# Performance work log

Measured on AMD Instinct MI355X. Metric: run time of the kernel, lower is better.

The kernel has to match this reference:

```python
import jax, jax.numpy as jnp
import numpy as np

# NCHW 3x3 conv, padding=1. BatchNorm (inference affine) is folded into conv weight/bias,
# which is mathematically identical to Conv->BN(eval) in the original.
def conv3(x, w, b, stride):
    y = jax.lax.conv_general_dilated(x, w, (stride, stride), [(1, 1), (1, 1)],
                                     dimension_numbers=('NCHW', 'OIHW', 'NCHW'))
    return y + b[None, :, None, None]

def lin1(x, w, b):  # 1x1 conv as channel matmul; w: [out, in]
    return jnp.einsum('oc,bchw->bohw', w, x) + b[None, :, None, None]

def setup_inputs():
    key = jax.random.key(0)
    ks = list(jax.random.split(key, 32))
    C, M = 32, 32  # cv_hypo_num, mid_dim (kq_dim == mid_dim since mid_dim <= 128)
    B, H, W = 1, 256, 512
    w3 = lambda k, o, i: jax.random.normal(k, (o, i, 3, 3), jnp.float32) * 0.05
    w1 = lambda k, o, i: jax.random.normal(k, (o, i), jnp.float32) * 0.05
    bv = lambda k, o: jax.random.normal(k, (o,), jnp.float32) * 0.01
    inp = {
        'mono_pseudo_cost': jax.random.normal(ks[0], (B, C, H, W), jnp.float32),
        'cost_volume': jax.random.normal(ks[1], (B, C, H, W), jnp.float32),
        # mono_expand / multi_expand: two stride-2 conv(+folded BN)+ReLU blocks each
        'me_w1': w3(ks[2], M, C), 'me_b1': bv(ks[3], M),
        'me_w2': w3(ks[4], M, C), 'me_b2': bv(ks[5], M),
        'xe_w1': w3(ks[6], M, C), 'xe_b1': bv(ks[7], M),
        'xe_w2': w3(ks[8], M, C), 'xe_b2': bv(ks[9], M),
        # 1x1 q/k/v projections for both branches
        'mq_w': w1(ks[10], M, M), 'mq_b': bv(ks[11], M),
        'mk_w': w1(ks[12], M, M), 'mk_b': bv(ks[13], M),
        'mv_w': w1(ks[14], M, M), 'mv_b': bv(ks[15], M),
        'xq_w': w1(ks[16], M, M), 'xq_b': bv(ks[17], M),
        'xk_w': w1(ks[18], M, M), 'xk_b': bv(ks[19], M),
        'xv_w': w1(ks[20], M, M), 'xv_b': bv(ks[21], M),
        # residual branches
        'mr_w1': w3(ks[22], M, C), 'mr_b1': bv(ks[23], M),
        'mr_w2': w3(ks[24], M, C), 'mr_b2': bv(ks[25], M),
        'xr_w': w1(ks[26], M, C), 'xr_b': bv(ks[27], M),
        'gamma': jnp.full((1,), 0.5, jnp.float32),  # nonzero so attention path is live
    }
    return inp

def reference(mono_pseudo_cost, cost_volume,
              me_w1, me_b1, me_w2, me_b2,
              xe_w1, xe_b1, xe_w2, xe_b2,
              mq_w, mq_b, mk_w, mk_b, mv_w, mv_b,
              xq_w, xq_b, xk_w, xk_b, xv_w, xv_b,
              mr_w1, mr_b1, mr_w2, mr_b2,
              xr_w, xr_b, gamma):
    relu = jax.nn.relu
    init_h, init_w = cost_volume.shape[2], cost_volume.shape[3]
    M = me_w1.shape[0]
    # feature extractors (stride-2 x2): [B,32,256,512] -> [B,32,64,128]
    mono_feat = relu(conv3(relu(conv3(mono_pseudo_cost, me_w1, me_b1, 2)), me_w2, me_b2, 2))
    multi_feat = relu(conv3(relu(conv3(cost_volume, xe_w1, xe_b1, 2)), xe_w2, xe_b2, 2))
    b, c, h, w = multi_feat.shape
    hw = h * w
    # q/k/v as [B, C, hw]
    mono_q = lin1(mono_feat, mq_w, mq_b).reshape(b, -1, hw)
    mono_k = lin1(mono_feat, mk_w, mk_b).reshape(b, -1, hw)
    mono_v = lin1(mono_feat, mv_w, mv_b).reshape(b, -1, hw)
    multi_q = lin1(multi_feat, xq_w, xq_b).reshape(b, -1, hw)
    multi_k = lin1(multi_feat, xk_w, xk_b).reshape(b, -1, hw)
    multi_v = lin1(multi_feat, xv_w, xv_b).reshape(b, -1, hw)
    # full [B, hw, hw] attention, no 1/sqrt(d) scaling (as in original)
    mono_atten = jax.nn.softmax(jnp.einsum('bci,bcj->bij', mono_q, mono_k), axis=-1)
    multi_atten = jax.nn.softmax(jnp.einsum('bci,bcj->bij', multi_q, multi_k), axis=-1)
    # cross application: mono values weighted by multi attention and vice versa
    mono_out = jnp.einsum('bcj,bij->bci', mono_v, multi_atten).reshape(b, M, h, w)
    multi_out = jnp.einsum('bcj,bij->bci', multi_v, mono_atten).reshape(b, M, h, w)
    fused = jnp.concatenate([multi_out, mono_out], axis=1)
    # nearest-neighbor upsample back to input size (integer factor 4)
    fused = jnp.repeat(jnp.repeat(fused, init_h // h, axis=2), init_w // w, axis=3)
    # residual branches
    mono_residual = relu(conv3(relu(conv3(mono_pseudo_cost, mr_w1, mr_b1, 1)), mr_w2, mr_b2, 1))
    multi_residual = relu(lin1(cost_volume, xr_w, xr_b))
    fused = jnp.concatenate([mono_residual, multi_residual], axis=1) + gamma * fused
    return fused
```

## Files before the change

### kernel.cpp

```cpp
#include <hip/hip_runtime.h>


using bf16x8 = __attribute__((ext_vector_type(8))) short;
using f32x4  = __attribute__((ext_vector_type(4))) float;
using f32x16 = __attribute__((ext_vector_type(16))) float;
typedef unsigned short u16;
typedef unsigned int   u32;

__device__ __forceinline__ u16 f2bf(float f) {
  u32 u = __builtin_bit_cast(u32, f);
  u = (u + 0x7fffu + ((u >> 16) & 1u)) >> 16;
  return (u16)u;
}
__device__ __forceinline__ float bf2f(u16 v) {
  u32 u = ((u32)v) << 16;
  return __builtin_bit_cast(float, u);
}
__device__ __forceinline__ u32 pktr(float lo, float hi) {
  return __builtin_amdgcn_perm(__builtin_bit_cast(u32, hi),
                               __builtin_bit_cast(u32, lo), 0x07060302u);
}
__device__ __forceinline__ f32x4 mfma16(bf16x8 a, bf16x8 b, f32x4 c) {
  return __builtin_amdgcn_mfma_f32_16x16x32_bf16(a, b, c, 0, 0, 0);
}
__device__ __forceinline__ f32x16 mfma32(bf16x8 a, bf16x8 b, f32x16 c) {
  return __builtin_amdgcn_mfma_f32_32x32x16_bf16(a, b, c, 0, 0, 0);
}
__device__ __forceinline__ f32x16 zero16() {
  f32x16 z = {0,0,0,0,0,0,0,0,0,0,0,0,0,0,0,0};
  return z;
}
__device__ __forceinline__ void store4bf(u16* dst, f32x4 v) {
  u32 lo = (u32)f2bf(v[0]) | ((u32)f2bf(v[1]) << 16);
  u32 hi = (u32)f2bf(v[2]) | ((u32)f2bf(v[3]) << 16);
  *(uint2*)dst = make_uint2(lo, hi);
}

struct WPtrs { const float* p[13]; };

__global__ void k_pre(WPtrs wp, u16* __restrict__ wConv, u16* __restrict__ w1x1,
                      const float* __restrict__ mono, const float* __restrict__ cv,
                      u16* __restrict__ monoT, u16* __restrict__ cvT,
                      u16* __restrict__ m1T, u16* __restrict__ x1T, u16* __restrict__ r1T) {
  int bx = blockIdx.x, t = threadIdx.x;
  if (bx < 13) {
    if (bx < 6) {
      const float* s = wp.p[bx];
      u16* d = wConv + bx * 9216;
      for (int i = t; i < 9216; i += 256) {
        int tap = i >> 10, co = (i >> 5) & 31, ci = i & 31;
        d[i] = f2bf(s[co * 288 + ci * 9 + tap]);
      }
    } else {
      const float* s = wp.p[bx];
      u16* d = w1x1 + (bx - 6) * 1024;
      for (int i = t; i < 1024; i += 256) d[i] = f2bf(s[i]);
    }
    return;
  }
  if (bx < 138) {
    int zb = bx - 13;
    int buf = zb % 5, blk = zb / 5;
    u16* b; int Hp, Wp;
    switch (buf) {
      case 0: b = monoT; Hp = 258; Wp = 514; break;
      case 1: b = cvT;   Hp = 258; Wp = 514; break;
      case 2: b = m1T;   Hp = 130; Wp = 258; break;
      case 3: b = x1T;   Hp = 130; Wp = 258; break;
      default: b = r1T;  Hp = 258; Wp = 514; break;
    }
    int id = blk * 256 + t;
    int cell = id >> 2, c8 = (id & 3) << 3;
    if (cell >= 2 * (Hp + Wp)) return;
    int r, c;
    if (cell < Wp)              { r = 0;                 c = cell; }
    else if (cell < 2 * Wp)     { r = Hp - 1;            c = cell - Wp; }
    else if (cell < 2 * Wp + Hp){ r = cell - 2 * Wp;     c = 0; }
    else                        { r = cell - 2 * Wp - Hp; c = Wp - 1; }
    bf16x8 z = {0, 0, 0, 0, 0, 0, 0, 0};
    *(bf16x8*)&b[(r * Wp + c) * 32 + c8] = z;
    return;
  }
  int idx = bx - 138;
  int xb = idx & 7, y = (idx >> 3) & 255, z = idx >> 11;
  const float* src = z ? cv : mono;
  u16* dst = z ? cvT : monoT;
  int x0 = xb << 6;
  __shared__ u16 tile[64][40];
  int ci = t >> 3, kx = (t & 7) << 3;
  const float* sp = src + ci * 131072 + y * 512 + x0 + kx;
  float4 a = *(const float4*)sp;
  float4 bb = *(const float4*)(sp + 4);
  tile[kx + 0][ci] = f2bf(a.x); tile[kx + 1][ci] = f2bf(a.y);
  tile[kx + 2][ci] = f2bf(a.z); tile[kx + 3][ci] = f2bf(a.w);
  tile[kx + 4][ci] = f2bf(bb.x); tile[kx + 5][ci] = f2bf(bb.y);
  tile[kx + 6][ci] = f2bf(bb.z); tile[kx + 7][ci] = f2bf(bb.w);
  __syncthreads();
  int x = t >> 2, c8 = (t & 3) << 3;
  bf16x8 v = *(bf16x8*)&tile[x][c8];
  *(bf16x8*)(dst + ((y + 1) * 514 + (x0 + x + 1)) * 32 + c8) = v;
}

__device__ __forceinline__ void conv3x3_body(int bxl, int tid,
    const u16* __restrict__ inT, int Wp, const u16* __restrict__ w9,
    const float* __restrict__ bias, u16* __restrict__ out, int outPitch,
    int outOff, int Ho, int tprShift, int stride) {
  int wid = (bxl * 256 + tid) >> 6;
  int lane = tid & 63, ln = lane & 15, q = lane >> 4;
  int y = wid >> tprShift;
  int x0 = (wid & ((1 << tprShift) - 1)) << 4;
  if (y >= Ho) return;
  f32x4 acc0 = *(const f32x4*)(bias + q * 4);
  f32x4 acc1 = *(const f32x4*)(bias + 16 + q * 4);
  const u16* ib = inT + (stride * y * Wp + stride * (x0 + ln)) * 32 + q * 8;
  const u16* wb = w9 + ln * 32 + q * 8;
#pragma unroll
  for (int dy = 0; dy < 3; ++dy)
#pragma unroll
    for (int dx = 0; dx < 3; ++dx) {
      int tap = dy * 3 + dx;
      bf16x8 bf = *(const bf16x8*)(ib + (dy * Wp + dx) * 32);
      acc0 = mfma16(*(const bf16x8*)(wb + tap * 1024), bf, acc0);
      acc1 = mfma16(*(const bf16x8*)(wb + tap * 1024 + 512), bf, acc1);
    }
#pragma unroll
  for (int r = 0; r < 4; ++r) { acc0[r] = fmaxf(acc0[r], 0.f); acc1[r] = fmaxf(acc1[r], 0.f); }
  u16* ob = out + (outOff + y * outPitch + x0 + ln) * 32;
  store4bf(ob + q * 4, acc0);
  store4bf(ob + 16 + q * 4, acc1);
}

__global__ void k_convs(const u16* __restrict__ monoT, const u16* __restrict__ cvT,
                        const u16* __restrict__ wConv,
                        const float* me_b1, const float* xe_b1, const float* mr_b1,
                        u16* __restrict__ m1T, u16* __restrict__ x1T, u16* __restrict__ r1T) {
  int bx = blockIdx.x;
  if (bx < 512)
    conv3x3_body(bx, threadIdx.x, monoT, 514, wConv + 0 * 9216, me_b1, m1T, 258, 259, 128, 4, 2);
  else if (bx < 1024)
    conv3x3_body(bx - 512, threadIdx.x, cvT, 514, wConv + 2 * 9216, xe_b1, x1T, 258, 259, 128, 4, 2);
  else
    conv3x3_body(bx - 1024, threadIdx.x, monoT, 514, wConv + 4 * 9216, mr_b1, r1T, 514, 515, 256, 5, 1);
}

__global__ void k_feat(const u16* __restrict__ m1T, const u16* __restrict__ x1T,
                       const u16* __restrict__ wConv,
                       const float* me_b2, const float* xe_b2,
                       u16* __restrict__ featM, u16* __restrict__ featX) {
  int bx = blockIdx.x;
  if (bx < 128)
    conv3x3_body(bx, threadIdx.x, m1T, 258, wConv + 1 * 9216, me_b2, featM, 128, 0, 64, 3, 2);
  else
    conv3x3_body(bx - 128, threadIdx.x, x1T, 258, wConv + 3 * 9216, xe_b2, featX, 128, 0, 64, 3, 2);
}

__global__ void k_proj(const u16* __restrict__ featM, const u16* __restrict__ featX,
                       const u16* __restrict__ w1x1,
                       const float* mq_b, const float* mk_b, const float* mv_b,
                       const float* xq_b, const float* xk_b, const float* xv_b,
                       u16* Qm, u16* Km, u16* Vm, u16* Qx, u16* Kx, u16* Vx) {
  int which = blockIdx.y;
  const u16* feat = (which < 3) ? featM : featX;
  const float* bias; u16* dst; float scale = 1.f; int cmode = 0;
  switch (which) {
    case 0: bias = mq_b; dst = Qm; scale = 1.4426950408889634f; break;
    case 1: bias = mk_b; dst = Km; break;
    case 2: bias = mv_b; dst = Vm; cmode = 1; break;
    case 3: bias = xq_b; dst = Qx; scale = 1.4426950408889634f; break;
    case 4: bias = xk_b; dst = Kx; break;
    default: bias = xv_b; dst = Vx; cmode = 1; break;
  }
  const u16* w = w1x1 + which * 1024;
  int wave = threadIdx.x >> 6, lane = threadIdx.x & 63, ln = lane & 15, q = lane >> 4;
  int p0 = (blockIdx.x * 4 + wave) << 4;
  bf16x8 bf = *(const bf16x8*)(feat + (p0 + ln) * 32 + q * 8);
  bf16x8 a0 = *(const bf16x8*)(w + ln * 32 + q * 8);
  bf16x8 a1 = *(const bf16x8*)(w + (16 + ln) * 32 + q * 8);
  f32x4 acc0 = *(const f32x4*)(bias + q * 4);
  f32x4 acc1 = *(const f32x4*)(bias + 16 + q * 4);
  acc0 = mfma16(a0, bf, acc0);
  acc1 = mfma16(a1, bf, acc1);
#pragma unroll
  for (int r = 0; r < 4; ++r) { acc0[r] *= scale; acc1[r] *= scale; }
  if (!cmode) {
    store4bf(dst + (p0 + ln) * 32 + q * 4, acc0);
    store4bf(dst + (p0 + ln) * 32 + 16 + q * 4, acc1);
  } else {
    int p = p0 + ln;
    int jl = p & 63, jb = p & ~63;
    int pj = jb + (jl >> 5) * 32 + ((jl >> 4) & 1) * 16 + ((jl >> 2) & 1) * 8
           + ((jl >> 3) & 1) * 4 + (jl & 3);
#pragma unroll
    for (int r = 0; r < 4; ++r) {
      dst[(q * 4 + r) * 8192 + pj] = f2bf(acc0[r]);
      dst[(16 + q * 4 + r) * 8192 + pj] = f2bf(acc1[r]);
    }
  }
}

__global__ void __launch_bounds__(256, 4) k_attention(
    const u16* __restrict__ Qm, const u16* __restrict__ Km, const u16* __restrict__ Vm,
    const u16* __restrict__ Qx, const u16* __restrict__ Kx, const u16* __restrict__ Vx,
    u16* __restrict__ Opart, float* __restrict__ lpart) {
  const u16 *Qp, *Kp, *Vp;
  int att = blockIdx.z;
  if (att == 0) { Qp = Qm; Kp = Km; Vp = Vx; }
  else          { Qp = Qx; Kp = Kx; Vp = Vm; }
  int sp = blockIdx.y;
  int j0 = sp << 10;

  __shared__ u16 Kl[2][64][40];
  __shared__ u16 Vl[2][32][72];

  int t = threadIdx.x, wave = t >> 6, lane = t & 63, ln = lane & 31, h = lane >> 5;
  int iw = blockIdx.x * 128 + wave * 32;

  bf16x8 qf0 = *(const bf16x8*)(Qp + (iw + ln) * 32 + h * 8);
  bf16x8 qf1 = *(const bf16x8*)(Qp + (iw + ln) * 32 + 16 + h * 8);

  int krow = t >> 2, kcol = (t & 3) << 3;
  int vrow = t >> 3, vcol = (t & 7) << 3;
  const u16* Kg = Kp + j0 * 32;
  const u16* Vg = Vp + j0;

  bf16x8 kn = *(const bf16x8*)(Kg + t * 8);
  bf16x8 vn = *(const bf16x8*)(Vg + vrow * 8192 + vcol);
  *(bf16x8*)&Kl[0][krow][kcol] = kn;
  *(bf16x8*)&Vl[0][vrow][vcol] = vn;

  f32x16 O = zero16(), lac = zero16();
  const short oneb = 0x3F80;
  const bf16x8 ones = {oneb, oneb, oneb, oneb, oneb, oneb, oneb, oneb};

  for (int jt = 0; jt < 16; ++jt) {
    __syncthreads();
    bool have = (jt + 1) < 16;
    if (have) {
      kn = *(const bf16x8*)(Kg + (jt + 1) * 2048 + t * 8);
      vn = *(const bf16x8*)(Vg + vrow * 8192 + (jt + 1) * 64 + vcol);
    }
    int cur = jt & 1;
    f32x16 s0 = mfma32(*(const bf16x8*)&Kl[cur][ln][h * 8], qf0, zero16());
    s0 = mfma32(*(const bf16x8*)&Kl[cur][ln][16 + h * 8], qf1, s0);
    f32x16 s1 = mfma32(*(const bf16x8*)&Kl[cur][32 + ln][h * 8], qf0, zero16());
    s1 = mfma32(*(const bf16x8*)&Kl[cur][32 + ln][16 + h * 8], qf1, s1);
    float e0[16], e1[16];
#pragma unroll
    for (int r = 0; r < 16; ++r) {
      e0[r] = __builtin_amdgcn_exp2f(s0[r]);
      e1[r] = __builtin_amdgcn_exp2f(s1[r]);
    }
    union PF { bf16x8 v; u32 w[4]; } pf[4];
#pragma unroll
    for (int t2 = 0; t2 < 4; ++t2) {
      int base = (t2 & 1) * 8;
      if (t2 < 2) {
#pragma unroll
        for (int p = 0; p < 4; ++p) pf[t2].w[p] = pktr(e0[base + 2 * p], e0[base + 2 * p + 1]);
      } else {
#pragma unroll
        for (int p = 0; p < 4; ++p) pf[t2].w[p] = pktr(e1[base + 2 * p], e1[base + 2 * p + 1]);
      }
    }
#pragma unroll
    for (int t2 = 0; t2 < 4; ++t2) {
      bf16x8 vf = *(const bf16x8*)&Vl[cur][ln][t2 * 16 + h * 8];
      O = mfma32(pf[t2].v, vf, O);
      lac = mfma32(pf[t2].v, ones, lac);
    }
    if (have) {
      *(bf16x8*)&Kl[1 - cur][krow][kcol] = kn;
      *(bf16x8*)&Vl[1 - cur][vrow][vcol] = vn;
    }
  }
  u16* ob = Opart + (size_t)(att * 8 + sp) * 262144;
  float* lb = lpart + (att * 8 + sp) * 8192;
#pragma unroll
  for (int r = 0; r < 16; ++r) {
    int ig = iw + (r & 3) + 8 * (r >> 2) + 4 * h;
    ob[ig * 32 + ln] = f2bf(O[r]);
    if (ln == 0) lb[ig] = lac[r];
  }
}

__global__ void k_reduce(const u16* __restrict__ Opart, const float* __restrict__ lpart,
                         float* __restrict__ attA, float* __restrict__ attB) {
  int a = blockIdx.y;
  int id = blockIdx.x * 256 + threadIdx.x;
  int i = id >> 5, c = id & 31;
  float s = 0.f, l = 0.f;
#pragma unroll
  for (int sp = 0; sp < 8; ++sp) {
    s += bf2f(Opart[(size_t)(a * 8 + sp) * 262144 + id]);
    l += lpart[(a * 8 + sp) * 8192 + i];
  }
  float* out = a ? attB : attA;
  out[i * 32 + c] = s / l;
}

__global__ void k_final(const u16* __restrict__ r1T, const u16* __restrict__ cvT,
                        const u16* __restrict__ wConv, const u16* __restrict__ w1x1,
                        const float* mr_b2, const float* xr_b,
                        const float* __restrict__ attA, const float* __restrict__ attB,
                        const float* __restrict__ gamma, float* __restrict__ dout) {
  int bx = blockIdx.x, tid = threadIdx.x;
  int lane = tid & 63, ln = lane & 15, q = lane >> 4;
  float g = gamma[0];
  if (bx < 2048) {
    const u16* w9 = wConv + 5 * 9216;
    int wid = (bx * 256 + tid) >> 6;
    int y = wid >> 5, x0 = (wid & 31) << 4;
    f32x4 acc0 = *(const f32x4*)(mr_b2 + q * 4);
    f32x4 acc1 = *(const f32x4*)(mr_b2 + 16 + q * 4);
    const u16* ib = r1T + (y * 514 + x0 + ln) * 32 + q * 8;
    const u16* wb = w9 + ln * 32 + q * 8;
#pragma unroll
    for (int dy = 0; dy < 3; ++dy)
#pragma unroll
      for (int dx = 0; dx < 3; ++dx) {
        int tap = dy * 3 + dx;
        bf16x8 bf = *(const bf16x8*)(ib + (dy * 514 + dx) * 32);
        acc0 = mfma16(*(const bf16x8*)(wb + tap * 1024), bf, acc0);
        acc1 = mfma16(*(const bf16x8*)(wb + tap * 1024 + 512), bf, acc1);
      }
    int xg = x0 + ln;
    const float* ap = attA + ((y >> 2) * 128 + (xg >> 2)) * 32;
    float* ob = dout + y * 512 + xg;
#pragma unroll
    for (int r = 0; r < 4; ++r) {
      int co0 = q * 4 + r, co1 = 16 + q * 4 + r;
      ob[co0 * 131072] = fmaxf(acc0[r], 0.f) + g * ap[co0];
      ob[co1 * 131072] = fmaxf(acc1[r], 0.f) + g * ap[co1];
    }
  } else {
    const u16* w = w1x1 + 6 * 1024;
    int wid = ((bx - 2048) * 256 + tid) >> 6;
    int p0 = wid << 4;
    int y = p0 >> 9, x0 = p0 & 511;
    bf16x8 bf = *(const bf16x8*)(cvT + ((y + 1) * 514 + x0 + ln + 1) * 32 + q * 8);
    f32x4 acc0 = *(const f32x4*)(xr_b + q * 4);
    f32x4 acc1 = *(const f32x4*)(xr_b + 16 + q * 4);
    acc0 = mfma16(*(const bf16x8*)(w + ln * 32 + q * 8), bf, acc0);
    acc1 = mfma16(*(const bf16x8*)(w + (16 + ln) * 32 + q * 8), bf, acc1);
    int xg = x0 + ln;
    const float* ap = attB + ((y >> 2) * 128 + (xg >> 2)) * 32;
    float* ob = dout + 32 * 131072 + p0 + ln;
#pragma unroll
    for (int r = 0; r < 4; ++r) {
      int co0 = q * 4 + r, co1 = 16 + q * 4 + r;
      ob[co0 * 131072] = fmaxf(acc0[r], 0.f) + g * ap[co0];
      ob[co1 * 131072] = fmaxf(acc1[r], 0.f) + g * ap[co1];
    }
  }
}

extern "C" void kernel_launch(void* const* d_in, const int* in_sizes, int n_in,
                              void* d_out, int out_size, void* d_ws, size_t ws_size,
                              hipStream_t stream) {
  const float* mono  = (const float*)d_in[0];
  const float* cv    = (const float*)d_in[1];
  const float* me_b1 = (const float*)d_in[3];
  const float* me_b2 = (const float*)d_in[5];
  const float* xe_b1 = (const float*)d_in[7];
  const float* xe_b2 = (const float*)d_in[9];
  const float* mq_b  = (const float*)d_in[11];
  const float* mk_b  = (const float*)d_in[13];
  const float* mv_b  = (const float*)d_in[15];
  const float* xq_b  = (const float*)d_in[17];
  const float* xk_b  = (const float*)d_in[19];
  const float* xv_b  = (const float*)d_in[21];
  const float* mr_b2 = (const float*)d_in[25];
  const float* mr_b1 = (const float*)d_in[23];
  const float* xr_b  = (const float*)d_in[27];
  const float* gamma = (const float*)d_in[28];
  float* dout = (float*)d_out;

  char* ws = (char*)d_ws;
  u16* wConv = (u16*)(ws + 0);
  u16* w1x1  = (u16*)(ws + 110592);
  u16* monoT = (u16*)(ws + 124928);
  u16* Opart = (u16*)(ws + 124928);
  u16* cvT   = (u16*)(ws + 8612096);
  u16* m1T   = (u16*)(ws + 17099264);
  u16* x1T   = (u16*)(ws + 19245824);
  u16* r1T   = (u16*)(ws + 21392384);
  u16* featM = (u16*)(ws + 29879552);
  u16* featX = (u16*)(ws + 30403840);
  u16* Qm    = (u16*)(ws + 30928128);
  u16* Km    = (u16*)(ws + 31452416);
  u16* Vm    = (u16*)(ws + 31976704);
  u16* Qx    = (u16*)(ws + 32500992);
  u16* Kx    = (u16*)(ws + 33025280);
  u16* Vx    = (u16*)(ws + 33549568);
  float* attA  = (float*)(ws + 34073856);
  float* attB  = (float*)(ws + 35122432);
  float* lpart = (float*)(ws + 36171008);

  WPtrs wp;
  wp.p[0] = (const float*)d_in[2];
  wp.p[1] = (const float*)d_in[4];
  wp.p[2] = (const float*)d_in[6];
  wp.p[3] = (const float*)d_in[8];
  wp.p[4] = (const float*)d_in[22];
  wp.p[5] = (const float*)d_in[24];
  wp.p[6] = (const float*)d_in[10];
  wp.p[7] = (const float*)d_in[12];
  wp.p[8] = (const float*)d_in[14];
  wp.p[9] = (const float*)d_in[16];
  wp.p[10] = (const float*)d_in[18];
  wp.p[11] = (const float*)d_in[20];
  wp.p[12] = (const float*)d_in[26];

  k_pre<<<4234, 256, 0, stream>>>(wp, wConv, w1x1, mono, cv, monoT, cvT, m1T, x1T, r1T);
  k_convs<<<3072, 256, 0, stream>>>(monoT, cvT, wConv, me_b1, xe_b1, mr_b1, m1T, x1T, r1T);
  k_feat<<<256, 256, 0, stream>>>(m1T, x1T, wConv, me_b2, xe_b2, featM, featX);
  k_proj<<<dim3(128, 6), 256, 0, stream>>>(featM, featX, w1x1,
                                           mq_b, mk_b, mv_b, xq_b, xk_b, xv_b,
                                           Qm, Km, Vm, Qx, Kx, Vx);
  k_attention<<<dim3(64, 8, 2), 256, 0, stream>>>(Qm, Km, Vm, Qx, Kx, Vx, Opart, lpart);
  k_reduce<<<dim3(1024, 2), 256, 0, stream>>>(Opart, lpart, attA, attB);
  k_final<<<4096, 256, 0, stream>>>(r1T, cvT, wConv, w1x1, mr_b2, xr_b, attA, attB, gamma, dout);
}
```

Baseline: 218.1 us.

## Fuse all stages into one persistent kernel with grid barriers

Replaces the seven separate kernel launches with a single persistent kernel that loops over the virtual blocks of each stage. Stages are separated by an atomic-counter grid barrier reset by a memset. The aim is to remove launch gaps and tail effects between the many short stages. Separately, the attention row-sum is now accumulated with scalar adds and a lane shuffle instead of an extra MFMA against a ones vector, and the exp work is interleaved with the second score MFMA. The risks are spin-barrier overhead, the hardcoded 256-CU grid assumption (deadlock if blocks are not co-resident), and occupancy limited by the largest stage's register use.

```diff
diff --git a/kernel.cpp b/kernel.cpp
--- a/kernel.cpp
+++ b/kernel.cpp
@@ -35,25 +35,52 @@
   u32 hi = (u32)f2bf(v[2]) | ((u32)f2bf(v[3]) << 16);
   *(uint2*)dst = make_uint2(lo, hi);
 }
-
-struct WPtrs { const float* p[13]; };
-
-__global__ void k_pre(WPtrs wp, u16* __restrict__ wConv, u16* __restrict__ w1x1,
-                      const float* __restrict__ mono, const float* __restrict__ cv,
-                      u16* __restrict__ monoT, u16* __restrict__ cvT,
-                      u16* __restrict__ m1T, u16* __restrict__ x1T, u16* __restrict__ r1T) {
-  int bx = blockIdx.x, t = threadIdx.x;
+__device__ __forceinline__ float sum16(const float* e) {
+  float s0 = e[0] + e[1], s1 = e[2] + e[3], s2 = e[4] + e[5], s3 = e[6] + e[7];
+  float s4 = e[8] + e[9], s5 = e[10] + e[11], s6 = e[12] + e[13], s7 = e[14] + e[15];
+  float a = s0 + s1, b = s2 + s3, c = s4 + s5, d = s6 + s7;
+  return (a + b) + (c + d);
+}
+
+struct UParams {
+  const float* wsrc[13];
+  const float *mono, *cv;
+  const float *me_b1, *xe_b1, *mr_b1, *me_b2, *xe_b2;
+  const float *mq_b, *mk_b, *mv_b, *xq_b, *xk_b, *xv_b;
+  const float *mr_b2, *xr_b, *gamma;
+  u16 *wConv, *w1x1, *monoT, *cvT, *m1T, *x1T, *r1T, *featM, *featX;
+  u16 *Qm, *Km, *Vm, *Qx, *Kx, *Vx, *Opart;
+  float *attA, *attB, *lpart, *dout;
+  unsigned* bar;
+};
+
+__device__ __forceinline__ void gsync(unsigned* bar, unsigned& ph) {
+  ++ph;
+  __syncthreads();
+  if (threadIdx.x == 0) {
+    __threadfence();
+    atomicAdd(bar, 1u);
+    unsigned tgt = ph * gridDim.x;
+    while (__hip_atomic_load(bar, __ATOMIC_RELAXED, __HIP_MEMORY_SCOPE_AGENT) < tgt)
+      __builtin_amdgcn_s_sleep(2);
+    __threadfence();
+  }
+  __syncthreads();
+}
+
+__device__ void pre_body(const UParams& Pp, int bx, char* smem) {
+  int t = threadIdx.x;
   if (bx < 13) {
     if (bx < 6) {
-      const float* s = wp.p[bx];
-      u16* d = wConv + bx * 9216;
+      const float* s = Pp.wsrc[bx];
+      u16* d = Pp.wConv + bx * 9216;
       for (int i = t; i < 9216; i += 256) {
         int tap = i >> 10, co = (i >> 5) & 31, ci = i & 31;
         d[i] = f2bf(s[co * 288 + ci * 9 + tap]);
       }
     } else {
-      const float* s = wp.p[bx];
-      u16* d = w1x1 + (bx - 6) * 1024;
+      const float* s = Pp.wsrc[bx];
+      u16* d = Pp.w1x1 + (bx - 6) * 1024;
       for (int i = t; i < 1024; i += 256) d[i] = f2bf(s[i]);
     }
     return;
@@ -63,11 +90,11 @@
     int buf = zb % 5, blk = zb / 5;
     u16* b; int Hp, Wp;
     switch (buf) {
-      case 0: b = monoT; Hp = 258; Wp = 514; break;
-      case 1: b = cvT;   Hp = 258; Wp = 514; break;
-      case 2: b = m1T;   Hp = 130; Wp = 258; break;
-      case 3: b = x1T;   Hp = 130; Wp = 258; break;
-      default: b = r1T;  Hp = 258; Wp = 514; break;
+      case 0: b = Pp.monoT; Hp = 258; Wp = 514; break;
+      case 1: b = Pp.cvT;   Hp = 258; Wp = 514; break;
+      case 2: b = Pp.m1T;   Hp = 130; Wp = 258; break;
+      case 3: b = Pp.x1T;   Hp = 130; Wp = 258; break;
+      default: b = Pp.r1T;  Hp = 258; Wp = 514; break;
     }
     int id = blk * 256 + t;
     int cell = id >> 2, c8 = (id & 3) << 3;
@@ -83,14 +110,15 @@
   }
   int idx = bx - 138;
   int xb = idx & 7, y = (idx >> 3) & 255, z = idx >> 11;
-  const float* src = z ? cv : mono;
-  u16* dst = z ? cvT : monoT;
+  const float* src = z ? Pp.cv : Pp.mono;
+  u16* dst = z ? Pp.cvT : Pp.monoT;
   int x0 = xb << 6;
-  __shared__ u16 tile[64][40];
+  u16 (*tile)[40] = (u16(*)[40])smem;
   int ci = t >> 3, kx = (t & 7) << 3;
   const float* sp = src + ci * 131072 + y * 512 + x0 + kx;
   float4 a = *(const float4*)sp;
   float4 bb = *(const float4*)(sp + 4);
+  __syncthreads();
   tile[kx + 0][ci] = f2bf(a.x); tile[kx + 1][ci] = f2bf(a.y);
   tile[kx + 2][ci] = f2bf(a.z); tile[kx + 3][ci] = f2bf(a.w);
   tile[kx + 4][ci] = f2bf(bb.x); tile[kx + 5][ci] = f2bf(bb.y);
@@ -130,49 +158,37 @@
   store4bf(ob + 16 + q * 4, acc1);
 }
 
-__global__ void k_convs(const u16* __restrict__ monoT, const u16* __restrict__ cvT,
-                        const u16* __restrict__ wConv,
-                        const float* me_b1, const float* xe_b1, const float* mr_b1,
-                        u16* __restrict__ m1T, u16* __restrict__ x1T, u16* __restrict__ r1T) {
-  int bx = blockIdx.x;
+__device__ void convs_body(const UParams& Pp, int bx) {
   if (bx < 512)
-    conv3x3_body(bx, threadIdx.x, monoT, 514, wConv + 0 * 9216, me_b1, m1T, 258, 259, 128, 4, 2);
+    conv3x3_body(bx, threadIdx.x, Pp.monoT, 514, Pp.wConv + 0 * 9216, Pp.me_b1, Pp.m1T, 258, 259, 128, 4, 2);
   else if (bx < 1024)
-    conv3x3_body(bx - 512, threadIdx.x, cvT, 514, wConv + 2 * 9216, xe_b1, x1T, 258, 259, 128, 4, 2);
+    conv3x3_body(bx - 512, threadIdx.x, Pp.cvT, 514, Pp.wConv + 2 * 9216, Pp.xe_b1, Pp.x1T, 258, 259, 128, 4, 2);
   else
-    conv3x3_body(bx - 1024, threadIdx.x, monoT, 514, wConv + 4 * 9216, mr_b1, r1T, 514, 515, 256, 5, 1);
-}
-
-__global__ void k_feat(const u16* __restrict__ m1T, const u16* __restrict__ x1T,
-                       const u16* __restrict__ wConv,
-                       const float* me_b2, const float* xe_b2,
-                       u16* __restrict__ featM, u16* __restrict__ featX) {
-  int bx = blockIdx.x;
+    conv3x3_body(bx - 1024, threadIdx.x, Pp.monoT, 514, Pp.wConv + 4 * 9216, Pp.mr_b1, Pp.r1T, 514, 515, 256, 5, 1);
+}
+
+__device__ void feat_body(const UParams& Pp, int bx) {
   if (bx < 128)
-    conv3x3_body(bx, threadIdx.x, m1T, 258, wConv + 1 * 9216, me_b2, featM, 128, 0, 64, 3, 2);
+    conv3x3_body(bx, threadIdx.x, Pp.m1T, 258, Pp.wConv + 1 * 9216, Pp.me_b2, Pp.featM, 128, 0, 64, 3, 2);
   else
-    conv3x3_body(bx - 128, threadIdx.x, x1T, 258, wConv + 3 * 9216, xe_b2, featX, 128, 0, 64, 3, 2);
-}
-
-__global__ void k_proj(const u16* __restrict__ featM, const u16* __restrict__ featX,
-                       const u16* __restrict__ w1x1,
-                       const float* mq_b, const float* mk_b, const float* mv_b,
-                       const float* xq_b, const float* xk_b, const float* xv_b,
-                       u16* Qm, u16* Km, u16* Vm, u16* Qx, u16* Kx, u16* Vx) {
-  int which = blockIdx.y;
-  const u16* feat = (which < 3) ? featM : featX;
+    conv3x3_body(bx - 128, threadIdx.x, Pp.x1T, 258, Pp.wConv + 3 * 9216, Pp.xe_b2, Pp.featX, 128, 0, 64, 3, 2);
+}
+
+__device__ void proj_body(const UParams& Pp, int vb) {
+  int which = vb >> 7, bxl = vb & 127;
+  const u16* feat = (which < 3) ? Pp.featM : Pp.featX;
   const float* bias; u16* dst; float scale = 1.f; int cmode = 0;
   switch (which) {
-    case 0: bias = mq_b; dst = Qm; scale = 1.4426950408889634f; break;
-    case 1: bias = mk_b; dst = Km; break;
-    case 2: bias = mv_b; dst = Vm; cmode = 1; break;
-    case 3: bias = xq_b; dst = Qx; scale = 1.4426950408889634f; break;
-    case 4: bias = xk_b; dst = Kx; break;
-    default: bias = xv_b; dst = Vx; cmode = 1; break;
-  }
-  const u16* w = w1x1 + which * 1024;
+    case 0: bias = Pp.mq_b; dst = Pp.Qm; scale = 1.4426950408889634f; break;
+    case 1: bias = Pp.mk_b; dst = Pp.Km; break;
+    case 2: bias = Pp.mv_b; dst = Pp.Vm; cmode = 1; break;
+    case 3: bias = Pp.xq_b; dst = Pp.Qx; scale = 1.4426950408889634f; break;
+    case 4: bias = Pp.xk_b; dst = Pp.Kx; break;
+    default: bias = Pp.xv_b; dst = Pp.Vx; cmode = 1; break;
+  }
+  const u16* w = Pp.w1x1 + which * 1024;
   int wave = threadIdx.x >> 6, lane = threadIdx.x & 63, ln = lane & 15, q = lane >> 4;
-  int p0 = (blockIdx.x * 4 + wave) << 4;
+  int p0 = (bxl * 4 + wave) << 4;
   bf16x8 bf = *(const bf16x8*)(feat + (p0 + ln) * 32 + q * 8);
   bf16x8 a0 = *(const bf16x8*)(w + ln * 32 + q * 8);
   bf16x8 a1 = *(const bf16x8*)(w + (16 + ln) * 32 + q * 8);
@@ -198,22 +214,20 @@
   }
 }
 
-__global__ void __launch_bounds__(256, 4) k_attention(
-    const u16* __restrict__ Qm, const u16* __restrict__ Km, const u16* __restrict__ Vm,
-    const u16* __restrict__ Qx, const u16* __restrict__ Kx, const u16* __restrict__ Vx,
-    u16* __restrict__ Opart, float* __restrict__ lpart) {
+__device__ void attn_body(const UParams& Pp, int vb, char* smem) {
+  int ib = vb & 63, sp = (vb >> 6) & 7, att = vb >> 9;
   const u16 *Qp, *Kp, *Vp;
-  int att = blockIdx.z;
-  if (att == 0) { Qp = Qm; Kp = Km; Vp = Vx; }
-  else          { Qp = Qx; Kp = Kx; Vp = Vm; }
-  int sp = blockIdx.y;
+  if (att == 0) { Qp = Pp.Qm; Kp = Pp.Km; Vp = Pp.Vx; }
+  else          { Qp = Pp.Qx; Kp = Pp.Kx; Vp = Pp.Vm; }
   int j0 = sp << 10;
 
-  __shared__ u16 Kl[2][64][40];
-  __shared__ u16 Vl[2][32][72];
+  typedef u16 KlT[64][40];
+  typedef u16 VlT[32][72];
+  KlT* Kl = (KlT*)smem;
+  VlT* Vl = (VlT*)(smem + 10240);
 
   int t = threadIdx.x, wave = t >> 6, lane = t & 63, ln = lane & 31, h = lane >> 5;
-  int iw = blockIdx.x * 128 + wave * 32;
+  int iw = ib * 128 + wave * 32;
 
   bf16x8 qf0 = *(const bf16x8*)(Qp + (iw + ln) * 32 + h * 8);
   bf16x8 qf1 = *(const bf16x8*)(Qp + (iw + ln) * 32 + 16 + h * 8);
@@ -225,12 +239,12 @@
 
   bf16x8 kn = *(const bf16x8*)(Kg + t * 8);
   bf16x8 vn = *(const bf16x8*)(Vg + vrow * 8192 + vcol);
+  __syncthreads();
   *(bf16x8*)&Kl[0][krow][kcol] = kn;
   *(bf16x8*)&Vl[0][vrow][vcol] = vn;
 
-  f32x16 O = zero16(), lac = zero16();
-  const short oneb = 0x3F80;
-  const bf16x8 ones = {oneb, oneb, oneb, oneb, oneb, oneb, oneb, oneb};
+  f32x16 O = zero16();
+  float lsum = 0.f;
 
   for (int jt = 0; jt < 16; ++jt) {
     __syncthreads();
@@ -240,24 +254,31 @@
       vn = *(const bf16x8*)(Vg + vrow * 8192 + (jt + 1) * 64 + vcol);
     }
     int cur = jt & 1;
+    union PF { bf16x8 v; u32 w[4]; } pf[4];
     f32x16 s0 = mfma32(*(const bf16x8*)&Kl[cur][ln][h * 8], qf0, zero16());
     s0 = mfma32(*(const bf16x8*)&Kl[cur][ln][16 + h * 8], qf1, s0);
+    {
+      float e0[16];
+#pragma unroll
+      for (int r = 0; r < 16; ++r) e0[r] = __builtin_amdgcn_exp2f(s0[r]);
+      lsum += sum16(e0);
+#pragma unroll
+      for (int t2 = 0; t2 < 2; ++t2) {
+        int base = t2 * 8;
+#pragma unroll
+        for (int p = 0; p < 4; ++p) pf[t2].w[p] = pktr(e0[base + 2 * p], e0[base + 2 * p + 1]);
+      }
+    }
     f32x16 s1 = mfma32(*(const bf16x8*)&Kl[cur][32 + ln][h * 8], qf0, zero16());
     s1 = mfma32(*(const bf16x8*)&Kl[cur][32 + ln][16 + h * 8], qf1, s1);
-    float e0[16], e1[16];
-#pragma unroll
-    for (int r = 0; r < 16; ++r) {
-      e0[r] = __builtin_amdgcn_exp2f(s0[r]);
-      e1[r] = __builtin_amdgcn_exp2f(s1[r]);
-    }
-    union PF { bf16x8 v; u32 w[4]; } pf[4];
-#pragma unroll
-    for (int t2 = 0; t2 < 4; ++t2) {
-      int base = (t2 & 1) * 8;
-      if (t2 < 2) {
-#pragma unroll
-        for (int p = 0; p < 4; ++p) pf[t2].w[p] = pktr(e0[base + 2 * p], e0[base + 2 * p + 1]);
-      } else {
+    {
+      float e1[16];
+#pragma unroll
+      for (int r = 0; r < 16; ++r) e1[r] = __builtin_amdgcn_exp2f(s1[r]);
+      lsum += sum16(e1);
+#pragma unroll
+      for (int t2 = 2; t2 < 4; ++t2) {
+        int base = (t2 & 1) * 8;
 #pragma unroll
         for (int p = 0; p < 4; ++p) pf[t2].w[p] = pktr(e1[base + 2 * p], e1[base + 2 * p + 1]);
       }
@@ -266,53 +287,49 @@
     for (int t2 = 0; t2 < 4; ++t2) {
       bf16x8 vf = *(const bf16x8*)&Vl[cur][ln][t2 * 16 + h * 8];
       O = mfma32(pf[t2].v, vf, O);
-      lac = mfma32(pf[t2].v, ones, lac);
     }
     if (have) {
       *(bf16x8*)&Kl[1 - cur][krow][kcol] = kn;
       *(bf16x8*)&Vl[1 - cur][vrow][vcol] = vn;
     }
   }
-  u16* ob = Opart + (size_t)(att * 8 + sp) * 262144;
-  float* lb = lpart + (att * 8 + sp) * 8192;
+  u16* ob = Pp.Opart + (size_t)(att * 8 + sp) * 262144;
+  float* lb = Pp.lpart + (att * 8 + sp) * 8192;
 #pragma unroll
   for (int r = 0; r < 16; ++r) {
     int ig = iw + (r & 3) + 8 * (r >> 2) + 4 * h;
     ob[ig * 32 + ln] = f2bf(O[r]);
-    if (ln == 0) lb[ig] = lac[r];
-  }
-}
-
-__global__ void k_reduce(const u16* __restrict__ Opart, const float* __restrict__ lpart,
-                         float* __restrict__ attA, float* __restrict__ attB) {
-  int a = blockIdx.y;
-  int id = blockIdx.x * 256 + threadIdx.x;
-  int i = id >> 5, c = id & 31;
+  }
+  float lo = __shfl(lsum, lane ^ 32, 64);
+  float lt = lsum + lo;
+  if (lane < 32) lb[iw + lane] = lt;
+}
+
+__device__ void reduce_body(const UParams& Pp, int vb) {
+  int a = vb >> 10;
+  int id = (vb & 1023) * 256 + threadIdx.x;
+  int i = id >> 5;
   float s = 0.f, l = 0.f;
 #pragma unroll
   for (int sp = 0; sp < 8; ++sp) {
-    s += bf2f(Opart[(size_t)(a * 8 + sp) * 262144 + id]);
-    l += lpart[(a * 8 + sp) * 8192 + i];
-  }
-  float* out = a ? attB : attA;
-  out[i * 32 + c] = s / l;
-}
-
-__global__ void k_final(const u16* __restrict__ r1T, const u16* __restrict__ cvT,
-                        const u16* __restrict__ wConv, const u16* __restrict__ w1x1,
-                        const float* mr_b2, const float* xr_b,
-                        const float* __restrict__ attA, const float* __restrict__ attB,
-                        const float* __restrict__ gamma, float* __restrict__ dout) {
-  int bx = blockIdx.x, tid = threadIdx.x;
+    s += bf2f(Pp.Opart[(size_t)(a * 8 + sp) * 262144 + id]);
+    l += Pp.lpart[(a * 8 + sp) * 8192 + i];
+  }
+  float* out = a ? Pp.attB : Pp.attA;
+  out[id] = s / l;
+}
+
+__device__ void final_body(const UParams& Pp, int bx) {
+  int tid = threadIdx.x;
   int lane = tid & 63, ln = lane & 15, q = lane >> 4;
-  float g = gamma[0];
+  float g = Pp.gamma[0];
   if (bx < 2048) {
-    const u16* w9 = wConv + 5 * 9216;
+    const u16* w9 = Pp.wConv + 5 * 9216;
     int wid = (bx * 256 + tid) >> 6;
     int y = wid >> 5, x0 = (wid & 31) << 4;
-    f32x4 acc0 = *(const f32x4*)(mr_b2 + q * 4);
-    f32x4 acc1 = *(const f32x4*)(mr_b2 + 16 + q * 4);
-    const u16* ib = r1T + (y * 514 + x0 + ln) * 32 + q * 8;
+    f32x4 acc0 = *(const f32x4*)(Pp.mr_b2 + q * 4);
+    f32x4 acc1 = *(const f32x4*)(Pp.mr_b2 + 16 + q * 4);
+    const u16* ib = Pp.r1T + (y * 514 + x0 + ln) * 32 + q * 8;
     const u16* wb = w9 + ln * 32 + q * 8;
 #pragma unroll
     for (int dy = 0; dy < 3; ++dy)
@@ -324,8 +341,8 @@
         acc1 = mfma16(*(const bf16x8*)(wb + tap * 1024 + 512), bf, acc1);
       }
     int xg = x0 + ln;
-    const float* ap = attA + ((y >> 2) * 128 + (xg >> 2)) * 32;
-    float* ob = dout + y * 512 + xg;
+    const float* ap = Pp.attA + ((y >> 2) * 128 + (xg >> 2)) * 32;
+    float* ob = Pp.dout + y * 512 + xg;
 #pragma unroll
     for (int r = 0; r < 4; ++r) {
       int co0 = q * 4 + r, co1 = 16 + q * 4 + r;
@@ -333,18 +350,18 @@
       ob[co1 * 131072] = fmaxf(acc1[r], 0.f) + g * ap[co1];
     }
   } else {
-    const u16* w = w1x1 + 6 * 1024;
+    const u16* w = Pp.w1x1 + 6 * 1024;
     int wid = ((bx - 2048) * 256 + tid) >> 6;
     int p0 = wid << 4;
     int y = p0 >> 9, x0 = p0 & 511;
-    bf16x8 bf = *(const bf16x8*)(cvT + ((y + 1) * 514 + x0 + ln + 1) * 32 + q * 8);
-    f32x4 acc0 = *(const f32x4*)(xr_b + q * 4);
-    f32x4 acc1 = *(const f32x4*)(xr_b + 16 + q * 4);
+    bf16x8 bf = *(const bf16x8*)(Pp.cvT + ((y + 1) * 514 + x0 + ln + 1) * 32 + q * 8);
+    f32x4 acc0 = *(const f32x4*)(Pp.xr_b + q * 4);
+    f32x4 acc1 = *(const f32x4*)(Pp.xr_b + 16 + q * 4);
     acc0 = mfma16(*(const bf16x8*)(w + ln * 32 + q * 8), bf, acc0);
     acc1 = mfma16(*(const bf16x8*)(w + (16 + ln) * 32 + q * 8), bf, acc1);
     int xg = x0 + ln;
-    const float* ap = attB + ((y >> 2) * 128 + (xg >> 2)) * 32;
-    float* ob = dout + 32 * 131072 + p0 + ln;
+    const float* ap = Pp.attB + ((y >> 2) * 128 + (xg >> 2)) * 32;
+    float* ob = Pp.dout + 32 * 131072 + p0 + ln;
 #pragma unroll
     for (int r = 0; r < 4; ++r) {
       int co0 = q * 4 + r, co1 = 16 + q * 4 + r;
@@ -354,70 +371,91 @@
   }
 }
 
+__global__ void __launch_bounds__(256, 4) k_uber(UParams P) {
+  __shared__ char smem[19456] __attribute__((aligned(16)));
+  unsigned ph = 0;
+  int nb = gridDim.x, bid = blockIdx.x;
+
+  for (int vb = bid; vb < 4234; vb += nb) pre_body(P, vb, smem);
+  gsync(P.bar, ph);
+  for (int vb = bid; vb < 3072; vb += nb) convs_body(P, vb);
+  gsync(P.bar, ph);
+  for (int vb = bid; vb < 256; vb += nb) feat_body(P, vb);
+  gsync(P.bar, ph);
+  for (int vb = bid; vb < 768; vb += nb) proj_body(P, vb);
+  gsync(P.bar, ph);
+  for (int vb = bid; vb < 1024; vb += nb) attn_body(P, vb, smem);
+  gsync(P.bar, ph);
+  for (int vb = bid; vb < 2048; vb += nb) reduce_body(P, vb);
+  gsync(P.bar, ph);
+  for (int vb = bid; vb < 4096; vb += nb) final_body(P, vb);
+}
+
 extern "C" void kernel_launch(void* const* d_in, const int* in_sizes, int n_in,
                               void* d_out, int out_size, void* d_ws, size_t ws_size,
                               hipStream_t stream) {
-  const float* mono  = (const float*)d_in[0];
-  const float* cv    = (const float*)d_in[1];
-  const float* me_b1 = (const float*)d_in[3];
-  const float* me_b2 = (const float*)d_in[5];
-  const float* xe_b1 = (const float*)d_in[7];
-  const float* xe_b2 = (const float*)d_in[9];
-  const float* mq_b  = (const float*)d_in[11];
-  const float* mk_b  = (const float*)d_in[13];
-  const float* mv_b  = (const float*)d_in[15];
-  const float* xq_b  = (const float*)d_in[17];
-  const float* xk_b  = (const float*)d_in[19];
-  const float* xv_b  = (const float*)d_in[21];
-  const float* mr_b2 = (const float*)d_in[25];
-  const float* mr_b1 = (const float*)d_in[23];
-  const float* xr_b  = (const float*)d_in[27];
-  const float* gamma = (const float*)d_in[28];
-  float* dout = (float*)d_out;
-
   char* ws = (char*)d_ws;
-  u16* wConv = (u16*)(ws + 0);
-  u16* w1x1  = (u16*)(ws + 110592);
-  u16* monoT = (u16*)(ws + 124928);
-  u16* Opart = (u16*)(ws + 124928);
-  u16* cvT   = (u16*)(ws + 8612096);
-  u16* m1T   = (u16*)(ws + 17099264);
-  u16* x1T   = (u16*)(ws + 19245824);
-  u16* r1T   = (u16*)(ws + 21392384);
-  u16* featM = (u16*)(ws + 29879552);
-  u16* featX = (u16*)(ws + 30403840);
-  u16* Qm    = (u16*)(ws + 30928128);
-  u16* Km    = (u16*)(ws + 31452416);
-  u16* Vm    = (u16*)(ws + 31976704);
-  u16* Qx    = (u16*)(ws + 32500992);
-  u16* Kx    = (u16*)(ws + 33025280);
-  u16* Vx    = (u16*)(ws + 33549568);
-  float* attA  = (float*)(ws + 34073856);
-  float* attB  = (float*)(ws + 35122432);
-  float* lpart = (float*)(ws + 36171008);
-
-  WPtrs wp;
-  wp.p[0] = (const float*)d_in[2];
-  wp.p[1] = (const float*)d_in[4];
-  wp.p[2] = (const float*)d_in[6];
-  wp.p[3] = (const float*)d_in[8];
-  wp.p[4] = (const float*)d_in[22];
-  wp.p[5] = (const float*)d_in[24];
-  wp.p[6] = (const float*)d_in[10];
-  wp.p[7] = (const float*)d_in[12];
-  wp.p[8] = (const float*)d_in[14];
-  wp.p[9] = (const float*)d_in[16];
-  wp.p[10] = (const float*)d_in[18];
-  wp.p[11] = (const float*)d_in[20];
-  wp.p[12] = (const float*)d_in[26];
-
-  k_pre<<<4234, 256, 0, stream>>>(wp, wConv, w1x1, mono, cv, monoT, cvT, m1T, x1T, r1T);
-  k_convs<<<3072, 256, 0, stream>>>(monoT, cvT, wConv, me_b1, xe_b1, mr_b1, m1T, x1T, r1T);
-  k_feat<<<256, 256, 0, stream>>>(m1T, x1T, wConv, me_b2, xe_b2, featM, featX);
-  k_proj<<<dim3(128, 6), 256, 0, stream>>>(featM, featX, w1x1,
-                                           mq_b, mk_b, mv_b, xq_b, xk_b, xv_b,
-                                           Qm, Km, Vm, Qx, Kx, Vx);
-  k_attention<<<dim3(64, 8, 2), 256, 0, stream>>>(Qm, Km, Vm, Qx, Kx, Vx, Opart, lpart);
-  k_reduce<<<dim3(1024, 2), 256, 0, stream>>>(Opart, lpart, attA, attB);
-  k_final<<<4096, 256, 0, stream>>>(r1T, cvT, wConv, w1x1, mr_b2, xr_b, attA, attB, gamma, dout);
-}
+  UParams P;
+  P.mono  = (const float*)d_in[0];
+  P.cv    = (const float*)d_in[1];
+  P.me_b1 = (const float*)d_in[3];
+  P.me_b2 = (const float*)d_in[5];
+  P.xe_b1 = (const float*)d_in[7];
+  P.xe_b2 = (const float*)d_in[9];
+  P.mq_b  = (const float*)d_in[11];
+  P.mk_b  = (const float*)d_in[13];
+  P.mv_b  = (const float*)d_in[15];
+  P.xq_b  = (const float*)d_in[17];
+  P.xk_b  = (const float*)d_in[19];
+  P.xv_b  = (const float*)d_in[21];
+  P.mr_b1 = (const float*)d_in[23];
+  P.mr_b2 = (const float*)d_in[25];
+  P.xr_b  = (const float*)d_in[27];
+  P.gamma = (const float*)d_in[28];
+  P.dout  = (float*)d_out;
+
+  P.wConv = (u16*)(ws + 0);
+  P.w1x1  = (u16*)(ws + 110592);
+  P.monoT = (u16*)(ws + 124928);
+  P.Opart = (u16*)(ws + 124928);
+  P.cvT   = (u16*)(ws + 8612096);
+  P.m1T   = (u16*)(ws + 17099264);
+  P.x1T   = (u16*)(ws + 19245824);
+  P.r1T   = (u16*)(ws + 21392384);
+  P.featM = (u16*)(ws + 29879552);
+  P.featX = (u16*)(ws + 30403840);
+  P.Qm    = (u16*)(ws + 30928128);
+  P.Km    = (u16*)(ws + 31452416);
+  P.Vm    = (u16*)(ws + 31976704);
+  P.Qx    = (u16*)(ws + 32500992);
+  P.Kx    = (u16*)(ws + 33025280);
+  P.Vx    = (u16*)(ws + 33549568);
+  P.attA  = (float*)(ws + 34073856);
+  P.attB  = (float*)(ws + 35122432);
+  P.lpart = (float*)(ws + 36171008);
+  P.bar   = (unsigned*)(ws + 36695296);
+
+  P.wsrc[0] = (const float*)d_in[2];
+  P.wsrc[1] = (const float*)d_in[4];
+  P.wsrc[2] = (const float*)d_in[6];
+  P.wsrc[3] = (const float*)d_in[8];
+  P.wsrc[4] = (const float*)d_in[22];
+  P.wsrc[5] = (const float*)d_in[24];
+  P.wsrc[6] = (const float*)d_in[10];
+  P.wsrc[7] = (const float*)d_in[12];
+  P.wsrc[8] = (const float*)d_in[14];
+  P.wsrc[9] = (const float*)d_in[16];
+  P.wsrc[10] = (const float*)d_in[18];
+  P.wsrc[11] = (const float*)d_in[20];
+  P.wsrc[12] = (const float*)d_in[26];
+
+  hipMemsetAsync(P.bar, 0, 64, stream);
+
+  int maxb = 0;
+  hipOccupancyMaxActiveBlocksPerMultiprocessor(&maxb, k_uber, 256, 0);
+  if (maxb <= 0) maxb = 2;
+  if (maxb > 4) maxb = 4;
+  int nb = maxb * 256;
+
+  k_uber<<<dim3(nb), dim3(256), 0, stream>>>(P);
+}
```

Result: slower. 522.8 us (+139.8%).
